# Optimization experiments

Measured on AMD Instinct MI355X. Metric: run time of the kernel, lower is better.

The kernel has to match this reference:

```python
import jax, jax.numpy as jnp
import numpy as np

B = 1048576
CONV_THRESHOLD = 0.0

def setup_inputs() -> dict:
    key = jax.random.key(0)
    ks = jax.random.split(key, 24)
    g = lambda i, shape, scale=0.3: (jax.random.normal(ks[i], shape, dtype=jnp.float32) * scale)
    return {
        "x": jax.random.normal(ks[0], (B, 2), dtype=jnp.float32),
        # photonic-style fraud net: 4 layers of tanh(W h + b), 2->2
        "fraud_W": g(1, (4, 2, 2), 0.8),
        "fraud_b": g(2, (4, 2), 0.1),
        # autoencoder encoder: 2 -> 64 -> 32 -> 8
        "enc_W1": g(3, (64, 2)), "enc_b1": g(4, (64,), 0.05),
        "enc_W2": g(5, (32, 64)), "enc_b2": g(6, (32,), 0.05),
        "enc_W3": g(7, (8, 32)), "enc_b3": g(8, (8,), 0.05),
        # decoder: 8 -> 32 -> 64 -> 2
        "dec_W1": g(9, (32, 8)), "dec_b1": g(10, (32,), 0.05),
        "dec_W2": g(11, (64, 32)), "dec_b2": g(12, (64,), 0.05),
        "dec_W3": g(13, (2, 64)), "dec_b3": g(14, (2,), 0.05),
        # quantum-like 2x2 conv filter (classical surrogate)
        "conv_k": g(15, (2, 2), 0.5),
        # sampler QNN: 2 -> 4 -> 2 + softmax
        "s_W1": g(16, (4, 2), 0.8), "s_b1": g(17, (4,), 0.1),
        "s_W2": g(18, (2, 4), 0.8), "s_b2": g(19, (2,), 0.1),
    }

def reference(x, fraud_W, fraud_b, enc_W1, enc_b1, enc_W2, enc_b2, enc_W3, enc_b3,
              dec_W1, dec_b1, dec_W2, dec_b2, dec_W3, dec_b3,
              conv_k, s_W1, s_b1, s_W2, s_b2):
    # fraud_net: stacked 2x2 affine + tanh layers
    h = x
    for i in range(fraud_W.shape[0]):
        h = jnp.tanh(h @ fraud_W[i].T + fraud_b[i])  # [B,2]
    # autoencoder encode / decode (eval mode: dropout is identity)
    z1 = jax.nn.relu(h @ enc_W1.T + enc_b1)          # [B,64]
    z2 = jax.nn.relu(z1 @ enc_W2.T + enc_b2)         # [B,32]
    latent = z2 @ enc_W3.T + enc_b3                  # [B,8]
    d1 = jax.nn.relu(latent @ dec_W1.T + dec_b1)     # [B,32]
    d2 = jax.nn.relu(d1 @ dec_W2.T + dec_b2)         # [B,64]
    recon = d2 @ dec_W3.T + dec_b3                   # [B,2] (unused downstream, as in original)
    # batched replacement of the per-sample CPU conv loop
    patch = jnp.stack([h[:, 0], h[:, 1], h[:, 0], h[:, 1]], axis=1).reshape(-1, 2, 2)
    conv_out = jax.nn.sigmoid(jnp.sum(patch * conv_k, axis=(1, 2)) - CONV_THRESHOLD)  # [B]
    inp = jnp.concatenate([h[:, 0:1], conv_out[:, None]], axis=-1)  # [B,2]
    logits = jnp.tanh(inp @ s_W1.T + s_b1) @ s_W2.T + s_b2
    return jax.nn.softmax(logits, axis=-1)           # [B,2]
```

## Files before the change

kernel.cpp:

```cpp
#include <hip/hip_runtime.h>


#define LOG2E 1.44269504088896f

__device__ __forceinline__ float frcp(float x) { return __builtin_amdgcn_rcpf(x); }

__device__ __forceinline__ float ftanh(float x) {
    return 1.0f - 2.0f * frcp(exp2f(2.0f * LOG2E * x) + 1.0f);
}

__global__ __launch_bounds__(256) void fraud_fused_kernel(
    const float4* __restrict__ x,
    float4* __restrict__ out,
    const float* __restrict__ fW,
    const float* __restrict__ fb,
    const float* __restrict__ ck,
    const float* __restrict__ sW1,
    const float* __restrict__ sb1,
    const float* __restrict__ sW2,
    const float* __restrict__ sb2,
    int nquads)
{
    int i = blockIdx.x * blockDim.x + threadIdx.x;
    if (i >= nquads) return;

    float W[16];
    #pragma unroll
    for (int k = 0; k < 16; ++k) W[k] = fW[k];
    float bb[8];
    #pragma unroll
    for (int k = 0; k < 8; ++k) bb[k] = fb[k];
    const float ck0 = ck[0] + ck[2];
    const float ck1 = ck[1] + ck[3];
    float w1[8];
    #pragma unroll
    for (int k = 0; k < 8; ++k) w1[k] = sW1[k];
    float b1[4];
    #pragma unroll
    for (int k = 0; k < 4; ++k) b1[k] = sb1[k];
    float w2[8];
    #pragma unroll
    for (int k = 0; k < 8; ++k) w2[k] = sW2[k];
    const float b20 = sb2[0], b21 = sb2[1];

    float4 xv0 = x[2 * i + 0];
    float4 xv1 = x[2 * i + 1];
    float hx[4] = {xv0.x, xv0.z, xv1.x, xv1.z};
    float hy[4] = {xv0.y, xv0.w, xv1.y, xv1.w};
    float r[8];

    #pragma unroll
    for (int s = 0; s < 4; ++s) {
        float h0 = hx[s], h1 = hy[s];

        #pragma unroll
        for (int l = 0; l < 4; ++l) {
            float a0 = fmaf(h0, W[4*l + 0], fmaf(h1, W[4*l + 1], bb[2*l + 0]));
            float a1 = fmaf(h0, W[4*l + 2], fmaf(h1, W[4*l + 3], bb[2*l + 1]));
            h0 = ftanh(a0);
            h1 = ftanh(a1);
        }

        float cs = fmaf(h0, ck0, h1 * ck1);
        float conv = frcp(1.0f + exp2f(-LOG2E * cs));

        float t0 = ftanh(fmaf(h0, w1[0], fmaf(conv, w1[1], b1[0])));
        float t1 = ftanh(fmaf(h0, w1[2], fmaf(conv, w1[3], b1[1])));
        float t2 = ftanh(fmaf(h0, w1[4], fmaf(conv, w1[5], b1[2])));
        float t3 = ftanh(fmaf(h0, w1[6], fmaf(conv, w1[7], b1[3])));

        float l0 = fmaf(t0, w2[0], fmaf(t1, w2[1], fmaf(t2, w2[2], fmaf(t3, w2[3], b20))));
        float l1 = fmaf(t0, w2[4], fmaf(t1, w2[5], fmaf(t2, w2[6], fmaf(t3, w2[7], b21))));

        float e  = exp2f(LOG2E * (l1 - l0));
        float p0 = frcp(1.0f + e);
        r[2*s + 0] = p0;
        r[2*s + 1] = 1.0f - p0;
    }

    out[2 * i + 0] = make_float4(r[0], r[1], r[2], r[3]);
    out[2 * i + 1] = make_float4(r[4], r[5], r[6], r[7]);
}

extern "C" void kernel_launch(void* const* d_in, const int* in_sizes, int n_in,
                              void* d_out, int out_size, void* d_ws, size_t ws_size,
                              hipStream_t stream) {
    const float4* x  = (const float4*)d_in[0];
    const float* fW  = (const float*)d_in[1];
    const float* fb  = (const float*)d_in[2];
    const float* ck  = (const float*)d_in[15];
    const float* sW1 = (const float*)d_in[16];
    const float* sb1 = (const float*)d_in[17];
    const float* sW2 = (const float*)d_in[18];
    const float* sb2 = (const float*)d_in[19];
    float4* out = (float4*)d_out;

    const int B = in_sizes[0] / 2;
    const int nquads = B / 4;
    const int block = 256;
    const int grid = (nquads + block - 1) / block;

    fraud_fused_kernel<<<grid, block, 0, stream>>>(
        x, out, fW, fb, ck, sW1, sb1, sW2, sb2, nquads);
}
```

Before: 102.1 us.

## Fold softmax difference weights, use raw exp2 intrinsic, nontemporal I/O, two samples per thread

```diff
diff --git a/kernel.cpp b/kernel.cpp
--- a/kernel.cpp
+++ b/kernel.cpp
@@ -3,15 +3,18 @@
 
 #define LOG2E 1.44269504088896f
 
-__device__ __forceinline__ float frcp(float x) { return __builtin_amdgcn_rcpf(x); }
+typedef float v4f __attribute__((ext_vector_type(4)));
+
+__device__ __forceinline__ float frcp(float x)  { return __builtin_amdgcn_rcpf(x); }
+__device__ __forceinline__ float fexp2(float x) { return __builtin_amdgcn_exp2f(x); }
 
 __device__ __forceinline__ float ftanh(float x) {
-    return 1.0f - 2.0f * frcp(exp2f(2.0f * LOG2E * x) + 1.0f);
+    return 1.0f - 2.0f * frcp(fexp2(2.0f * LOG2E * x) + 1.0f);
 }
 
 __global__ __launch_bounds__(256) void fraud_fused_kernel(
-    const float4* __restrict__ x,
-    float4* __restrict__ out,
+    const v4f* __restrict__ x,
+    v4f* __restrict__ out,
     const float* __restrict__ fW,
     const float* __restrict__ fb,
     const float* __restrict__ ck,
@@ -19,10 +22,10 @@
     const float* __restrict__ sb1,
     const float* __restrict__ sW2,
     const float* __restrict__ sb2,
-    int nquads)
+    int n)
 {
     int i = blockIdx.x * blockDim.x + threadIdx.x;
-    if (i >= nquads) return;
+    if (i >= n) return;
 
     float W[16];
     #pragma unroll
@@ -30,27 +33,27 @@
     float bb[8];
     #pragma unroll
     for (int k = 0; k < 8; ++k) bb[k] = fb[k];
-    const float ck0 = ck[0] + ck[2];
-    const float ck1 = ck[1] + ck[3];
+    const float ckx = -LOG2E * (ck[0] + ck[2]);
+    const float cky = -LOG2E * (ck[1] + ck[3]);
     float w1[8];
     #pragma unroll
     for (int k = 0; k < 8; ++k) w1[k] = sW1[k];
     float b1[4];
     #pragma unroll
     for (int k = 0; k < 4; ++k) b1[k] = sb1[k];
-    float w2[8];
-    #pragma unroll
-    for (int k = 0; k < 8; ++k) w2[k] = sW2[k];
-    const float b20 = sb2[0], b21 = sb2[1];
+    const float dw0 = LOG2E * (sW2[4] - sW2[0]);
+    const float dw1 = LOG2E * (sW2[5] - sW2[1]);
+    const float dw2 = LOG2E * (sW2[6] - sW2[2]);
+    const float dw3 = LOG2E * (sW2[7] - sW2[3]);
+    const float db  = LOG2E * (sb2[1] - sb2[0]);
 
-    float4 xv0 = x[2 * i + 0];
-    float4 xv1 = x[2 * i + 1];
-    float hx[4] = {xv0.x, xv0.z, xv1.x, xv1.z};
-    float hy[4] = {xv0.y, xv0.w, xv1.y, xv1.w};
-    float r[8];
+    v4f xv = __builtin_nontemporal_load(x + i);
+    float hx[2] = {xv.x, xv.z};
+    float hy[2] = {xv.y, xv.w};
+    float r[4];
 
     #pragma unroll
-    for (int s = 0; s < 4; ++s) {
+    for (int s = 0; s < 2; ++s) {
         float h0 = hx[s], h1 = hy[s];
 
         #pragma unroll
@@ -61,31 +64,28 @@
             h1 = ftanh(a1);
         }
 
-        float cs = fmaf(h0, ck0, h1 * ck1);
-        float conv = frcp(1.0f + exp2f(-LOG2E * cs));
+        float conv = frcp(1.0f + fexp2(fmaf(h0, ckx, h1 * cky)));
 
         float t0 = ftanh(fmaf(h0, w1[0], fmaf(conv, w1[1], b1[0])));
         float t1 = ftanh(fmaf(h0, w1[2], fmaf(conv, w1[3], b1[1])));
         float t2 = ftanh(fmaf(h0, w1[4], fmaf(conv, w1[5], b1[2])));
         float t3 = ftanh(fmaf(h0, w1[6], fmaf(conv, w1[7], b1[3])));
 
-        float l0 = fmaf(t0, w2[0], fmaf(t1, w2[1], fmaf(t2, w2[2], fmaf(t3, w2[3], b20))));
-        float l1 = fmaf(t0, w2[4], fmaf(t1, w2[5], fmaf(t2, w2[6], fmaf(t3, w2[7], b21))));
-
-        float e  = exp2f(LOG2E * (l1 - l0));
-        float p0 = frcp(1.0f + e);
+        float d  = fmaf(t0, dw0, fmaf(t1, dw1, fmaf(t2, dw2, fmaf(t3, dw3, db))));
+        float p0 = frcp(1.0f + fexp2(d));
         r[2*s + 0] = p0;
         r[2*s + 1] = 1.0f - p0;
     }
 
-    out[2 * i + 0] = make_float4(r[0], r[1], r[2], r[3]);
-    out[2 * i + 1] = make_float4(r[4], r[5], r[6], r[7]);
+    v4f o;
+    o.x = r[0]; o.y = r[1]; o.z = r[2]; o.w = r[3];
+    __builtin_nontemporal_store(o, out + i);
 }
 
 extern "C" void kernel_launch(void* const* d_in, const int* in_sizes, int n_in,
                               void* d_out, int out_size, void* d_ws, size_t ws_size,
                               hipStream_t stream) {
-    const float4* x  = (const float4*)d_in[0];
+    const v4f* x     = (const v4f*)d_in[0];
     const float* fW  = (const float*)d_in[1];
     const float* fb  = (const float*)d_in[2];
     const float* ck  = (const float*)d_in[15];
@@ -93,13 +93,12 @@
     const float* sb1 = (const float*)d_in[17];
     const float* sW2 = (const float*)d_in[18];
     const float* sb2 = (const float*)d_in[19];
-    float4* out = (float4*)d_out;
+    v4f* out = (v4f*)d_out;
 
-    const int B = in_sizes[0] / 2;
-    const int nquads = B / 4;
+    const int n = in_sizes[0] / 4;
     const int block = 256;
-    const int grid = (nquads + block - 1) / block;
+    const int grid = (n + block - 1) / block;
 
     fraud_fused_kernel<<<grid, block, 0, stream>>>(
-        x, out, fW, fb, ck, sW1, sb1, sW2, sb2, nquads);
+        x, out, fW, fb, ck, sW1, sb1, sW2, sb2, n);
 }
```

Result: no change. 101.0 us (-1.1%).
